# Kernel tuning notes

Hardware: AMD Instinct MI355X
Metric: run time of the kernel (lower is better)

## Reference

```python
import jax, jax.numpy as jnp
import numpy as np

ACOSH_MIN = 1.0 + 1e-07
ACOSH_MAX = 50.0
TEMP_EPS = 1e-08


def setup_inputs() -> dict:
    key = jax.random.key(0)
    k1, k2 = jax.random.split(key)
    B, S, D = 8, 2048, 65  # manifold_dim = dim + 1 for hyperbolic (Lorentz)
    x = jax.random.normal(k1, (B, S, D), dtype=jnp.float32)
    values = jax.random.normal(k2, (B, S, D), dtype=jnp.float32)
    temperature = jnp.float32(1.0)  # nn.Parameter initialized to 1.0
    return {"x": x, "values": values, "temperature": temperature}


def reference(x, values, temperature):
    # Lorentz (hyperbolic) pairwise inner product:
    # <x_i, x_j>_L = -x_i[0]*x_j[0] + sum_k x_i[k]*x_j[k], k>=1
    time_product = -jnp.einsum('bs,bt->bst', x[..., 0], x[..., 0])
    space_product = jnp.einsum('bsd,btd->bst', x[..., 1:], x[..., 1:])
    lorentz_product = time_product + space_product  # [B,S,S]
    acosh_input = jnp.clip(-lorentz_product, ACOSH_MIN, ACOSH_MAX)
    distances = jnp.arccosh(acosh_input)
    scores = -distances / (temperature + TEMP_EPS)
    attention = jax.nn.softmax(scores, axis=-1)  # [B,S,S]
    output = jnp.einsum('bst,btd->bsd', attention, values)
    return (output, attention)
```

## Files before the change

kernel.cpp:

```cpp
#include <hip/hip_runtime.h>
#include <math.h>

constexpr int NB = 8, NS = 2048, ND = 65;
constexpr int KX = 64;
constexpr int LP = 68;
constexpr int VD = 80;
constexpr size_t OUTSZ = (size_t)NB * NS * ND;
constexpr size_t CONVN = (size_t)NB * NS * KX;
constexpr size_t VTN   = (size_t)NB * VD * NS;

typedef short short8 __attribute__((ext_vector_type(8)));
typedef float f32x4 __attribute__((ext_vector_type(4)));

union S8U { short8 v; ushort4 h[2]; };
__device__ __forceinline__ short8 ld8(const ushort* p) {
    S8U u; u.h[0] = *(const ushort4*)p; u.h[1] = *(const ushort4*)(p + 4); return u.v;
}

__device__ __forceinline__ ushort f2bf(float f) {
    uint u = __float_as_uint(f);
    return (ushort)((u + 0x7fffu + ((u >> 16) & 1u)) >> 16);
}
__device__ __forceinline__ float bf2f(ushort h) {
    return __uint_as_float((uint)h << 16);
}

__global__ __launch_bounds__(256)
void k0_convert(const float* __restrict__ x, ushort* __restrict__ xhi,
                ushort* __restrict__ xlo, float* __restrict__ x64)
{
    int i = blockIdx.x * 256 + threadIdx.x;
    int row = i >> 3, g = i & 7;
    if (row >= NB * NS) return;
    int d0 = g * 8;
    short8 vh, vl;
    #pragma unroll
    for (int e = 0; e < 8; ++e) {
        float v = x[(size_t)row * ND + d0 + e];
        ushort h = f2bf(v);
        vh[e] = (short)h;
        vl[e] = (short)f2bf(v - bf2f(h));
    }
    *(short8*)&xhi[(size_t)row * KX + d0] = vh;
    *(short8*)&xlo[(size_t)row * KX + d0] = vl;
    if (g == 0) x64[row] = x[(size_t)row * ND + 64];
}

__global__ __launch_bounds__(256)
void k0v_transpose(const float* __restrict__ v, ushort* __restrict__ vthi)
{
    __shared__ float sT[32][66];
    const int tid = threadIdx.x, b = blockIdx.y, t0 = blockIdx.x * 32;
    const float* vb = v + (size_t)b * NS * ND;
    for (int i = tid; i < 32 * ND; i += 256) {
        int t = i / ND, d = i - t * ND;
        sT[t][d] = vb[(size_t)(t0 + t) * ND + d];
    }
    __syncthreads();
    for (int i = tid; i < VD * 32; i += 256) {
        int d = i >> 5, t = i & 31;
        float val = (d < ND) ? sT[t][d] : 0.0f;
        vthi[((size_t)b * VD + d) * NS + t0 + t] = f2bf(val);
    }
}

__global__ __launch_bounds__(512, 4)
void k1u_scores(const ushort* __restrict__ xhi, const ushort* __restrict__ xlo,
                const float* __restrict__ x64, const float* __restrict__ tptr,
                ushort* __restrict__ eg, float* __restrict__ rsp)
{
    __shared__ __align__(16) ushort sAh[64 * LP], sAl[64 * LP];
    __shared__ __align__(16) ushort sBh[128 * LP], sBl[128 * LP];
    __shared__ __align__(16) float sB64[128];

    const int tid = threadIdx.x;
    const int f  = (blockIdx.x & 7) * 64 + (blockIdx.x >> 3);
    const int b  = f >> 6;
    const int rblk = (f >> 1) & 31;
    const int ch = f & 1;
    const int r0 = rblk * 64;
    const int tc0 = ch * (NS / 2);
    const int lane = tid & 63;
    const int q = lane >> 4, c = lane & 15;
    const int w  = tid >> 6;
    const int wr = w >> 2;
    const int wc = w & 3;
    const float invT = 1.0f / (tptr[0] + 1e-8f);
    const bool fastT = (invT == 1.0f);

    const ushort* xhb = xhi + (size_t)b * NS * KX;
    const ushort* xlb = xlo + (size_t)b * NS * KX;
    const float*  x64b = x64 + (size_t)b * NS;
    ushort* erow = eg + ((size_t)b * NS + r0) * NS;

    for (int i = tid; i < 64 * 8; i += 512) {
        int row = i >> 3, g = i & 7;
        uint4 vh = *(const uint4*)&xhb[(size_t)(r0 + row) * KX + g * 8];
        uint4 vl = *(const uint4*)&xlb[(size_t)(r0 + row) * KX + g * 8];
        int so = row * LP + g * 8;
        *(uint2*)&sAh[so]     = make_uint2(vh.x, vh.y);
        *(uint2*)&sAh[so + 4] = make_uint2(vh.z, vh.w);
        *(uint2*)&sAl[so]     = make_uint2(vl.x, vl.y);
        *(uint2*)&sAl[so + 4] = make_uint2(vl.z, vl.w);
    }
    __syncthreads();
    if (tid < 64) { sAh[tid * LP] ^= 0x8000; sAl[tid * LP] ^= 0x8000; }

    float a64r[2];
    #pragma unroll
    for (int rf = 0; rf < 2; ++rf)
        a64r[rf] = x64b[r0 + wr * 32 + rf * 16 + c];

    float rsum[2] = {0.0f, 0.0f};

    for (int tcl = 0; tcl < NS / 2; tcl += 128) {
        const int tc = tc0 + tcl;
        __syncthreads();
        for (int i = tid; i < 128 * 8; i += 512) {
            int row = i >> 3, g = i & 7;
            uint4 vh = *(const uint4*)&xhb[(size_t)(tc + row) * KX + g * 8];
            uint4 vl = *(const uint4*)&xlb[(size_t)(tc + row) * KX + g * 8];
            int so = row * LP + g * 8;
            *(uint2*)&sBh[so]     = make_uint2(vh.x, vh.y);
            *(uint2*)&sBh[so + 4] = make_uint2(vh.z, vh.w);
            *(uint2*)&sBl[so]     = make_uint2(vl.x, vl.y);
            *(uint2*)&sBl[so + 4] = make_uint2(vl.z, vl.w);
        }
        if (tid < 128) sB64[tid] = x64b[tc + tid];
        __syncthreads();

        f32x4 acc[2][2];
        #pragma unroll
        for (int rf = 0; rf < 2; ++rf)
            #pragma unroll
            for (int cf = 0; cf < 2; ++cf)
                #pragma unroll
                for (int j = 0; j < 4; ++j) acc[rf][cf][j] = 0.0f;

        #pragma unroll
        for (int kc = 0; kc < 2; ++kc) {
            const int koff = kc * 32 + q * 8;
            short8 ah[2], al[2], bh[2], bl[2];
            #pragma unroll
            for (int rf = 0; rf < 2; ++rf) {
                int ro = (wr * 32 + rf * 16 + c) * LP + koff;
                ah[rf] = ld8(&sAh[ro]);
                al[rf] = ld8(&sAl[ro]);
            }
            #pragma unroll
            for (int cf = 0; cf < 2; ++cf) {
                int co = (wc * 32 + cf * 16 + c) * LP + koff;
                bh[cf] = ld8(&sBh[co]);
                bl[cf] = ld8(&sBl[co]);
            }
            #pragma unroll
            for (int rf = 0; rf < 2; ++rf)
                #pragma unroll
                for (int cf = 0; cf < 2; ++cf) {
                    acc[rf][cf] = __builtin_amdgcn_mfma_f32_16x16x32_bf16(bh[cf], ah[rf], acc[rf][cf], 0, 0, 0);
                    acc[rf][cf] = __builtin_amdgcn_mfma_f32_16x16x32_bf16(bl[cf], ah[rf], acc[rf][cf], 0, 0, 0);
                    acc[rf][cf] = __builtin_amdgcn_mfma_f32_16x16x32_bf16(bh[cf], al[rf], acc[rf][cf], 0, 0, 0);
                }
        }

        #pragma unroll
        for (int rf = 0; rf < 2; ++rf) {
            const int row = wr * 32 + rf * 16 + c;
            #pragma unroll
            for (int cf = 0; cf < 2; ++cf) {
                float4 b64v = *(const float4*)&sB64[wc * 32 + cf * 16 + q * 4];
                float e4[4];
                #pragma unroll
                for (int j = 0; j < 4; ++j) {
                    float bj = (j == 0) ? b64v.x : (j == 1) ? b64v.y
                             : (j == 2) ? b64v.z : b64v.w;
                    float accf = acc[rf][cf][j] + a64r[rf] * bj;
                    float z = -accf;
                    z = fminf(fmaxf(z, 1.0000001f), 50.0f);
                    float s = __fsqrt_rn(z * z - 1.0f);
                    float e = fastT ? (z - s)
                                    : __expf(-__logf(z + s) * invT);
                    e4[j] = e;
                    rsum[rf] += e;
                }
                ushort4 pk = make_ushort4(
                    (ushort)__float2uint_rn(e4[0] * 65535.0f),
                    (ushort)__float2uint_rn(e4[1] * 65535.0f),
                    (ushort)__float2uint_rn(e4[2] * 65535.0f),
                    (ushort)__float2uint_rn(e4[3] * 65535.0f));
                *(ushort4*)&erow[(size_t)row * NS + tc + wc * 32 + cf * 16 + q * 4] = pk;
            }
        }
    }

    __syncthreads();
    float* sSum = (float*)sBh;
    #pragma unroll
    for (int rf = 0; rf < 2; ++rf) {
        float v = rsum[rf];
        v += __shfl_xor(v, 16, 64);
        v += __shfl_xor(v, 32, 64);
        if (q == 0) sSum[wc * 64 + wr * 32 + rf * 16 + c] = v;
    }
    __syncthreads();
    if (tid < 64)
        rsp[(size_t)ch * NB * NS + (size_t)b * NS + r0 + tid] =
            sSum[tid] + sSum[64 + tid] + sSum[128 + tid] + sSum[192 + tid];
}

__global__ __launch_bounds__(256)
void k1b_inv(const float* __restrict__ rsp, float* __restrict__ invb)
{
    int i = blockIdx.x * 256 + threadIdx.x;
    invb[i] = 1.0f / (rsp[i] + rsp[(size_t)NB * NS + i]);
}

__global__ __launch_bounds__(512, 4)
void k2u_pv(const ushort* __restrict__ eg, const ushort* __restrict__ vthi,
            const float* __restrict__ invb, float* __restrict__ attn,
            float* __restrict__ out)
{
    __shared__ __align__(16) char smem[40960];
    ushort* sAh = (ushort*)smem;
    ushort* sAl = sAh + 32 * 136;
    ushort* sVh = sAl + 32 * 136;
    float*  sInvL = (float*)(smem + 39168);
    float*  sRed = (float*)smem;

    const int tid = threadIdx.x;
    const int f  = (blockIdx.x & 7) * 64 + (blockIdx.x >> 3);
    const int b  = f >> 6;
    const int r0 = (f & 63) * 32;
    const int lane = tid & 63;
    const int q = lane >> 4, c = lane & 15;
    const int w = tid >> 6;
    const int wk = w & 3;
    const int rfh = w >> 2;

    if (tid < 32) sInvL[tid] = invb[(size_t)b * NS + r0 + tid] * (1.0f / 65535.0f);

    const ushort* erow = eg + ((size_t)b * NS + r0) * NS;
    float* arow = attn + ((size_t)b * NS + r0) * NS;
    const ushort* vh = vthi + (size_t)b * VD * NS;

    short8 ereg;
    short8 vregh[3];
    auto loadE = [&](int kt) {
        int row = tid >> 4, c8 = tid & 15;
        ereg = *(const short8*)&erow[(size_t)row * NS + kt + c8 * 8];
    };
    auto loadV = [&](int kt) {
        #pragma unroll
        for (int rep = 0; rep < 3; ++rep) {
            int i = tid + rep * 512;
            if (i < VD * 16) {
                int d = i >> 4, c8 = i & 15;
                vregh[rep] = *(const short8*)&vh[(size_t)d * NS + kt + c8 * 8];
            }
        }
    };

    f32x4 acc[5];
    #pragma unroll
    for (int ff = 0; ff < 5; ++ff)
        #pragma unroll
        for (int j = 0; j < 4; ++j) acc[ff][j] = 0.0f;

    loadE(0);
    loadV(0);
    __syncthreads();

    for (int kt = 0; kt < NS; kt += 128) {
        {
            int row = tid >> 4, c8 = tid & 15;
            float inv2 = sInvL[row];
            float en[8];
            #pragma unroll
            for (int i = 0; i < 8; ++i)
                en[i] = (float)(ushort)ereg[i] * inv2;
            float4 fa = {en[0], en[1], en[2], en[3]};
            float4 fb = {en[4], en[5], en[6], en[7]};
            *(float4*)&arow[(size_t)row * NS + kt + c8 * 8]     = fa;
            *(float4*)&arow[(size_t)row * NS + kt + c8 * 8 + 4] = fb;
            ushort h[8], l[8];
            #pragma unroll
            for (int i = 0; i < 8; ++i) {
                h[i] = f2bf(en[i]);
                l[i] = f2bf(en[i] - bf2f(h[i]));
            }
            int so = row * 136 + c8 * 8;
            *(ushort4*)&sAh[so]     = make_ushort4(h[0], h[1], h[2], h[3]);
            *(ushort4*)&sAh[so + 4] = make_ushort4(h[4], h[5], h[6], h[7]);
            *(ushort4*)&sAl[so]     = make_ushort4(l[0], l[1], l[2], l[3]);
            *(ushort4*)&sAl[so + 4] = make_ushort4(l[4], l[5], l[6], l[7]);
        }
        #pragma unroll
        for (int rep = 0; rep < 3; ++rep) {
            int i = tid + rep * 512;
            if (i < VD * 16) {
                int d = i >> 4, c8 = i & 15;
                *(short8*)&sVh[d * 136 + c8 * 8] = vregh[rep];
            }
        }
        __syncthreads();

        if (kt + 128 < NS) { loadE(kt + 128); loadV(kt + 128); }

        const int koff = wk * 32 + q * 8;
        short8 ah = *(const short8*)&sAh[(rfh * 16 + c) * 136 + koff];
        short8 al = *(const short8*)&sAl[(rfh * 16 + c) * 136 + koff];
        #pragma unroll
        for (int ff = 0; ff < 5; ++ff) {
            short8 bh = *(const short8*)&sVh[(ff * 16 + c) * 136 + koff];
            acc[ff] = __builtin_amdgcn_mfma_f32_16x16x32_bf16(ah, bh, acc[ff], 0, 0, 0);
            acc[ff] = __builtin_amdgcn_mfma_f32_16x16x32_bf16(al, bh, acc[ff], 0, 0, 0);
        }
        __syncthreads();
    }

    #pragma unroll
    for (int ff = 0; ff < 5; ++ff)
        #pragma unroll
        for (int j = 0; j < 4; ++j) {
            int r = rfh * 16 + q * 4 + j;
            int d = ff * 16 + c;
            sRed[((size_t)wk * 32 + r) * 80 + d] = acc[ff][j];
        }
    __syncthreads();
    for (int i = tid; i < 32 * 80; i += 512) {
        int r = i / 80, d = i - r * 80;
        float s = sRed[i] + sRed[2560 + i] + sRed[5120 + i] + sRed[7680 + i];
        if (d < ND) out[((size_t)b * NS + r0 + r) * ND + d] = s;
    }
}

extern "C" void kernel_launch(void* const* d_in, const int* in_sizes, int n_in,
                              void* d_out, int out_size, void* d_ws, size_t ws_size,
                              hipStream_t stream) {
    const float* x      = (const float*)d_in[0];
    const float* values = (const float*)d_in[1];
    const float* temp   = (const float*)d_in[2];

    float* out  = (float*)d_out;
    float* attn = out + OUTSZ;

    ushort* xhi  = (ushort*)d_ws;
    ushort* xlo  = xhi + CONVN;
    ushort* vthi = xlo + CONVN;
    float*  x64  = (float*)(vthi + VTN);
    float*  invb = x64 + (size_t)NB * NS;
    float*  rsp  = invb + (size_t)NB * NS;
    ushort* eg   = (ushort*)(rsp + 2 * (size_t)NB * NS);

    k0_convert<<<(NB * NS * 8) / 256, 256, 0, stream>>>(x, xhi, xlo, x64);
    k0v_transpose<<<dim3(NS / 32, NB), 256, 0, stream>>>(values, vthi);

    k1u_scores<<<512, 512, 0, stream>>>(xhi, xlo, x64, temp, eg, rsp);
    k1b_inv<<<NB * NS / 256, 256, 0, stream>>>(rsp, invb);
    k2u_pv<<<512, 512, 0, stream>>>(eg, vthi, invb, attn, out);
}
```

Baseline: 82.15 us.

## Register-prefetch next B tile in scores kernel and fold inverse-sum kernel into PV

The scores kernel now loads the next 128-row block of converted x (hi/lo bf16 plus time component) into registers while the MFMA work on the current tile runs, then writes those registers to shared memory at the start of the next iteration. This hides global load latency behind compute at the cost of extra VGPRs, which could lower occupancy. The small k1b_inv kernel is removed and its reciprocal of the two partial row sums is computed directly in k2u_pv, saving one launch and one round trip through global memory.

Result: faster. 79.34 us (-3.4%).

```diff
diff --git a/kernel.cpp b/kernel.cpp
--- a/kernel.cpp
+++ b/kernel.cpp
@@ -93,6 +93,21 @@
     const float*  x64b = x64 + (size_t)b * NS;
     ushort* erow = eg + ((size_t)b * NS + r0) * NS;
 
+    uint4 pbh[2], pbl[2];
+    float pb64;
+    auto loadB = [&](int tc) {
+        #pragma unroll
+        for (int r = 0; r < 2; ++r) {
+            int i = tid + r * 512;
+            int row = i >> 3, g = i & 7;
+            pbh[r] = *(const uint4*)&xhb[(size_t)(tc + row) * KX + g * 8];
+            pbl[r] = *(const uint4*)&xlb[(size_t)(tc + row) * KX + g * 8];
+        }
+        if (tid < 128) pb64 = x64b[tc + tid];
+    };
+
+    loadB(tc0);
+
     for (int i = tid; i < 64 * 8; i += 512) {
         int row = i >> 3, g = i & 7;
         uint4 vh = *(const uint4*)&xhb[(size_t)(r0 + row) * KX + g * 8];
@@ -116,18 +131,20 @@
     for (int tcl = 0; tcl < NS / 2; tcl += 128) {
         const int tc = tc0 + tcl;
         __syncthreads();
-        for (int i = tid; i < 128 * 8; i += 512) {
+        #pragma unroll
+        for (int r = 0; r < 2; ++r) {
+            int i = tid + r * 512;
             int row = i >> 3, g = i & 7;
-            uint4 vh = *(const uint4*)&xhb[(size_t)(tc + row) * KX + g * 8];
-            uint4 vl = *(const uint4*)&xlb[(size_t)(tc + row) * KX + g * 8];
             int so = row * LP + g * 8;
-            *(uint2*)&sBh[so]     = make_uint2(vh.x, vh.y);
-            *(uint2*)&sBh[so + 4] = make_uint2(vh.z, vh.w);
-            *(uint2*)&sBl[so]     = make_uint2(vl.x, vl.y);
-            *(uint2*)&sBl[so + 4] = make_uint2(vl.z, vl.w);
-        }
-        if (tid < 128) sB64[tid] = x64b[tc + tid];
+            *(uint2*)&sBh[so]     = make_uint2(pbh[r].x, pbh[r].y);
+            *(uint2*)&sBh[so + 4] = make_uint2(pbh[r].z, pbh[r].w);
+            *(uint2*)&sBl[so]     = make_uint2(pbl[r].x, pbl[r].y);
+            *(uint2*)&sBl[so + 4] = make_uint2(pbl[r].z, pbl[r].w);
+        }
+        if (tid < 128) sB64[tid] = pb64;
         __syncthreads();
+
+        if (tcl + 128 < NS / 2) loadB(tc + 128);
 
         f32x4 acc[2][2];
         #pragma unroll
@@ -208,16 +225,9 @@
             sSum[tid] + sSum[64 + tid] + sSum[128 + tid] + sSum[192 + tid];
 }
 
-__global__ __launch_bounds__(256)
-void k1b_inv(const float* __restrict__ rsp, float* __restrict__ invb)
-{
-    int i = blockIdx.x * 256 + threadIdx.x;
-    invb[i] = 1.0f / (rsp[i] + rsp[(size_t)NB * NS + i]);
-}
-
 __global__ __launch_bounds__(512, 4)
 void k2u_pv(const ushort* __restrict__ eg, const ushort* __restrict__ vthi,
-            const float* __restrict__ invb, float* __restrict__ attn,
+            const float* __restrict__ rsp, float* __restrict__ attn,
             float* __restrict__ out)
 {
     __shared__ __align__(16) char smem[40960];
@@ -237,7 +247,10 @@
     const int wk = w & 3;
     const int rfh = w >> 2;
 
-    if (tid < 32) sInvL[tid] = invb[(size_t)b * NS + r0 + tid] * (1.0f / 65535.0f);
+    if (tid < 32) {
+        size_t i = (size_t)b * NS + r0 + tid;
+        sInvL[tid] = (1.0f / (rsp[i] + rsp[(size_t)NB * NS + i])) * (1.0f / 65535.0f);
+    }
 
     const ushort* erow = eg + ((size_t)b * NS + r0) * NS;
     float* arow = attn + ((size_t)b * NS + r0) * NS;
@@ -348,14 +361,12 @@
     ushort* xlo  = xhi + CONVN;
     ushort* vthi = xlo + CONVN;
     float*  x64  = (float*)(vthi + VTN);
-    float*  invb = x64 + (size_t)NB * NS;
-    float*  rsp  = invb + (size_t)NB * NS;
+    float*  rsp  = x64 + (size_t)NB * NS;
     ushort* eg   = (ushort*)(rsp + 2 * (size_t)NB * NS);
 
     k0_convert<<<(NB * NS * 8) / 256, 256, 0, stream>>>(x, xhi, xlo, x64);
     k0v_transpose<<<dim3(NS / 32, NB), 256, 0, stream>>>(values, vthi);
 
     k1u_scores<<<512, 512, 0, stream>>>(xhi, xlo, x64, temp, eg, rsp);
-    k1b_inv<<<NB * NS / 256, 256, 0, stream>>>(rsp, invb);
-    k2u_pv<<<512, 512, 0, stream>>>(eg, vthi, invb, attn, out);
-}
+    k2u_pv<<<512, 512, 0, stream>>>(eg, vthi, rsp, attn, out);
+}
```
